# Optimization experiments

Hardware: AMD Instinct MI355X
Metric: run time of the kernel (lower is better)

## Reference

```python
import jax, jax.numpy as jnp
import numpy as np

T, B, IN = 2048, 64, 256
H, L = 256, 3


def setup_inputs() -> dict:
    key = jax.random.key(0)
    ks = jax.random.split(key, 6)
    s = 1.0 / np.sqrt(H)  # torch default init scale
    return {
        "x": jax.random.normal(ks[0], (T, B, IN), dtype=jnp.float32),
        "h0": jax.random.normal(ks[1], (L, B, H), dtype=jnp.float32),
        "W_ih": jax.random.normal(ks[2], (L, 3 * H, IN), dtype=jnp.float32) * s,
        "W_hh": jax.random.normal(ks[3], (L, 3 * H, H), dtype=jnp.float32) * s,
        "b_ih": jax.random.normal(ks[4], (L, 3 * H), dtype=jnp.float32) * s,
        "b_hh": jax.random.normal(ks[5], (L, 3 * H), dtype=jnp.float32) * s,
    }


def _gru_layer(x, h0_l, Wih, Whh, bih, bhh):
    # Precompute input projections for all timesteps: [T, B, 3H]
    gx = jnp.einsum("tbi,gi->tbg", x, Wih) + bih

    def step(h, gx_t):
        gh = h @ Whh.T + bhh  # [B, 3H]
        xr, xz, xn = jnp.split(gx_t, 3, axis=-1)
        hr, hz, hn = jnp.split(gh, 3, axis=-1)
        r = jax.nn.sigmoid(xr + hr)
        z = jax.nn.sigmoid(xz + hz)
        n = jnp.tanh(xn + r * hn)
        h_new = (1.0 - z) * n + z * h
        return h_new, h_new

    hT, out = jax.lax.scan(step, h0_l, gx)
    return out, hT  # out: [T, B, H]


def reference(x, h0, W_ih, W_hh, b_ih, b_hh):
    inp = x
    h_n = []
    for l in range(L):
        inp, hT = _gru_layer(inp, h0[l], W_ih[l], W_hh[l], b_ih[l], b_hh[l])
        h_n.append(hT)
    return inp, jnp.stack(h_n, axis=0)
```

## Files before the change

kernel.cpp:

```cpp
#include <hip/hip_runtime.h>


typedef float  float4_  __attribute__((ext_vector_type(4)));
typedef short  short8_  __attribute__((ext_vector_type(8)));

#define DEVFN static __device__ __forceinline__

constexpr int T_ = 2048;
constexpr int B_ = 64;
constexpr int H_ = 256;
constexpr int G_ = 768;

DEVFN unsigned short f2bf(float f) {
  unsigned u = __float_as_uint(f);
  u += 0x7fffu + ((u >> 16) & 1u);
  return (unsigned short)(u >> 16);
}
DEVFN float bf2f(unsigned short s) { return __uint_as_float(((unsigned)s) << 16); }
DEVFN float rcp_(float x)  { return __builtin_amdgcn_rcpf(x); }
DEVFN float exp2_(float x) { return __builtin_amdgcn_exp2f(x); }
DEVFN float sigmoid_(float x) { return rcp_(1.f + exp2_(-1.4426950408889634f * x)); }
DEVFN float tanh_(float x)    { return 1.f - 2.f * rcp_(1.f + exp2_(2.8853900817779268f * x)); }

DEVFN void load_lds16(const void* g, void* l) {
  __builtin_amdgcn_global_load_lds(
      (__attribute__((address_space(1))) void*)g,
      (__attribute__((address_space(3))) void*)l, 16, 0, 0);
}

__global__ void convert_kernel(const float* __restrict__ x,
                               const float* __restrict__ wih,
                               const float* __restrict__ whh,
                               const float* __restrict__ bih,
                               const float* __restrict__ bhh,
                               unsigned short* __restrict__ xb,
                               unsigned short* __restrict__ wihb,
                               unsigned short* __restrict__ whhb,
                               float* __restrict__ biasf,
                               float* __restrict__ bhhn) {
  const long i0 = (long)blockIdx.x * blockDim.x + threadIdx.x;
  const long stride = (long)gridDim.x * blockDim.x;
  for (long i = i0; i < (long)T_ * B_ * H_; i += stride) xb[i] = f2bf(x[i]);
  for (long i = i0; i < 3L * G_ * H_; i += stride) {
    wihb[i] = f2bf(wih[i]);
    whhb[i] = f2bf(whh[i]);
  }
  for (long i = i0; i < 3L * G_; i += stride) {
    int g = (int)(i % G_);
    biasf[i] = bih[i] + (g < 512 ? bhh[i] : 0.f);
  }
  for (long i = i0; i < 3L * H_; i += stride) {
    int l = (int)(i >> 8), j = (int)(i & 255);
    bhhn[i] = bhh[l * G_ + 512 + j];
  }
}

__global__ __launch_bounds__(256) void gemm_gx(const unsigned short* __restrict__ A,
                                               const unsigned short* __restrict__ W,
                                               const float* __restrict__ bias,
                                               unsigned short* __restrict__ gxrz,
                                               float* __restrict__ gxn) {
  __shared__ alignas(16) unsigned short As[128 * 32];
  __shared__ alignas(16) unsigned short Bs[128 * 32];
  const int tid = threadIdx.x;
  const int bn = blockIdx.x;
  const size_t bm = blockIdx.y;
  const int wave = tid >> 6, lane = tid & 63;
  const int q = lane >> 4, nl = lane & 15;
  const int wr = (wave >> 1) * 64, wc = (wave & 1) * 64;
  const unsigned short* Ab = A + bm * 128 * 256;
  const unsigned short* Wb = W + (size_t)bn * 128 * 256;

  float4_ acc[4][4];
  float4_ z4 = {0.f, 0.f, 0.f, 0.f};
#pragma unroll
  for (int i = 0; i < 4; ++i)
#pragma unroll
    for (int j = 0; j < 4; ++j) acc[i][j] = z4;

  for (int kt = 0; kt < 8; ++kt) {
    const int k0 = kt * 32;
#pragma unroll
    for (int cc = 0; cc < 2; ++cc) {
      int ch = tid + 256 * cc;
      load_lds16(Ab + (size_t)(ch >> 2) * 256 + k0 + (ch & 3) * 8, &As[ch * 8]);
      load_lds16(Wb + (size_t)(ch >> 2) * 256 + k0 + (ch & 3) * 8, &Bs[ch * 8]);
    }
    __syncthreads();
    short8_ af[4], bf[4];
#pragma unroll
    for (int i = 0; i < 4; ++i) {
      af[i] = *(const short8_*)&As[(wr + i * 16 + nl) * 32 + q * 8];
      bf[i] = *(const short8_*)&Bs[(wc + i * 16 + nl) * 32 + q * 8];
    }
#pragma unroll
    for (int i = 0; i < 4; ++i)
#pragma unroll
      for (int j = 0; j < 4; ++j)
        acc[i][j] = __builtin_amdgcn_mfma_f32_16x16x32_bf16(af[i], bf[j], acc[i][j], 0, 0, 0);
    __syncthreads();
  }

  float bv[4];
#pragma unroll
  for (int j = 0; j < 4; ++j) bv[j] = bias[bn * 128 + wc + j * 16 + nl];

  if (bn < 4) {
#pragma unroll
    for (int i = 0; i < 4; ++i)
#pragma unroll
      for (int j = 0; j < 4; ++j) {
        const int gcol = bn * 128 + wc + j * 16 + nl;
#pragma unroll
        for (int r = 0; r < 4; ++r) {
          const size_t grow = bm * 128 + wr + i * 16 + q * 4 + r;
          gxrz[grow * 512 + gcol] = f2bf(acc[i][j][r] + bv[j]);
        }
      }
  } else {
#pragma unroll
    for (int i = 0; i < 4; ++i)
#pragma unroll
      for (int j = 0; j < 4; ++j) {
        const int gcol = bn * 128 + wc + j * 16 + nl;
#pragma unroll
        for (int r = 0; r < 4; ++r) {
          const size_t grow = bm * 128 + wr + i * 16 + q * 4 + r;
          gxn[grow * 256 + (gcol - 512)] = acc[i][j][r] + bv[j];
        }
      }
  }
}

__global__ __launch_bounds__(512, 2) void gru_layer(
    const unsigned short* __restrict__ gxrz,
    const float* __restrict__ gxn,
    const unsigned short* __restrict__ whh,
    const float* __restrict__ bhhn,
    const float* __restrict__ h0,
    unsigned short* __restrict__ outb,
    float* __restrict__ outf,
    float* __restrict__ hT) {
  __shared__ alignas(16) unsigned short h_bf[16][264];
  __shared__ float h_f[16][256];
  __shared__ alignas(16) unsigned short srz[16 * 512];
  __shared__ alignas(16) float sn[16 * 256];

  const int tid = threadIdx.x;
  const int rb = blockIdx.x * 16;
  const int wave = tid >> 6, lane = tid & 63;
  const int q = lane >> 4, nl = lane & 15;
  const int cb = wave * 32;

#pragma unroll
  for (int i = 0; i < 8; ++i) {
    int idx = tid + 512 * i, row = idx >> 8, col = idx & 255;
    float v = h0[(rb + row) * 256 + col];
    h_f[row][col] = v;
    h_bf[row][col] = f2bf(v);
  }

  short8_ wf[6][8];
#pragma unroll
  for (int c = 0; c < 2; ++c)
#pragma unroll
    for (int g = 0; g < 3; ++g) {
      const unsigned short* wrow = whh + (size_t)(g * 256 + cb + c * 16 + nl) * 256;
#pragma unroll
      for (int kt = 0; kt < 8; ++kt)
        wf[c * 3 + g][kt] = *(const short8_*)(wrow + kt * 32 + q * 8);
    }
  const float bn_[2] = { bhhn[cb + nl], bhhn[cb + 16 + nl] };

  {
    const unsigned short* s0 = gxrz + (size_t)rb * 512;
    const float* s1 = gxn + (size_t)rb * 256;
#pragma unroll
    for (int cc = 0; cc < 2; ++cc) {
      int ch = tid + 512 * cc;
      load_lds16(s0 + ch * 8, &srz[ch * 8]);
      load_lds16(s1 + ch * 4, &sn[ch * 4]);
    }
  }
  __syncthreads();

  for (int t = 0; t < T_; ++t) {
    float4_ acc[6];
    float4_ z4 = {0.f, 0.f, 0.f, 0.f};
#pragma unroll
    for (int u = 0; u < 6; ++u) acc[u] = z4;
#pragma unroll
    for (int kt = 0; kt < 8; ++kt) {
      short8_ af = *(const short8_*)&h_bf[nl][kt * 32 + q * 8];
#pragma unroll
      for (int u = 0; u < 6; ++u)
        acc[u] = __builtin_amdgcn_mfma_f32_16x16x32_bf16(af, wf[u][kt], acc[u], 0, 0, 0);
    }
    __syncthreads();

    float hnew[2][4];
#pragma unroll
    for (int c = 0; c < 2; ++c) {
      const int col = cb + c * 16 + nl;
#pragma unroll
      for (int r = 0; r < 4; ++r) {
        const int row = q * 4 + r;
        float xr = bf2f(srz[row * 512 + col]);
        float xz = bf2f(srz[row * 512 + 256 + col]);
        float xn = sn[row * 256 + col];
        float rr = sigmoid_(xr + acc[c * 3 + 0][r]);
        float zz = sigmoid_(xz + acc[c * 3 + 1][r]);
        float nn = tanh_(xn + rr * (acc[c * 3 + 2][r] + bn_[c]));
        float hold = h_f[row][col];
        float hv = nn + zz * (hold - nn);
        hnew[c][r] = hv;
        h_f[row][col] = hv;
        h_bf[row][col] = f2bf(hv);
      }
    }
    __syncthreads();

    const size_t ob = ((size_t)t * 64 + rb) * 256;
    if (outb) {
#pragma unroll
      for (int c = 0; c < 2; ++c)
#pragma unroll
        for (int r = 0; r < 4; ++r)
          outb[ob + (size_t)(q * 4 + r) * 256 + cb + c * 16 + nl] = f2bf(hnew[c][r]);
    }
    if (outf) {
#pragma unroll
      for (int c = 0; c < 2; ++c)
#pragma unroll
        for (int r = 0; r < 4; ++r)
          outf[ob + (size_t)(q * 4 + r) * 256 + cb + c * 16 + nl] = hnew[c][r];
    }
    if (t + 1 < T_) {
      const unsigned short* s0 = gxrz + ((size_t)(t + 1) * 64 + rb) * 512;
      const float* s1 = gxn + ((size_t)(t + 1) * 64 + rb) * 256;
#pragma unroll
      for (int cc = 0; cc < 2; ++cc) {
        int ch = tid + 512 * cc;
        load_lds16(s0 + ch * 8, &srz[ch * 8]);
        load_lds16(s1 + ch * 4, &sn[ch * 4]);
      }
    }
  }

#pragma unroll
  for (int i = 0; i < 8; ++i) {
    int idx = tid + 512 * i, row = idx >> 8, col = idx & 255;
    hT[(rb + row) * 256 + col] = h_f[row][col];
  }
}

extern "C" void kernel_launch(void* const* d_in, const int* in_sizes, int n_in,
                              void* d_out, int out_size, void* d_ws, size_t ws_size,
                              hipStream_t stream) {
  (void)in_sizes; (void)n_in; (void)out_size; (void)ws_size;
  const float* x   = (const float*)d_in[0];
  const float* h0  = (const float*)d_in[1];
  const float* wih = (const float*)d_in[2];
  const float* whh = (const float*)d_in[3];
  const float* bih = (const float*)d_in[4];
  const float* bhh = (const float*)d_in[5];
  float* out = (float*)d_out;
  char* ws = (char*)d_ws;

  unsigned short* gxrz = (unsigned short*)(ws + 0);
  float*          gxn  = (float*)(ws + 134217728);
  unsigned short* buf0 = (unsigned short*)(ws + 268435456);
  unsigned short* buf1 = (unsigned short*)(ws + 335544320);
  unsigned short* wihb = (unsigned short*)(ws + 402653184);
  unsigned short* whhb = (unsigned short*)(ws + 403832832);
  float*         biasf = (float*)(ws + 405012480);
  float*          bhhn = (float*)(ws + 405021696);

  convert_kernel<<<2048, 256, 0, stream>>>(x, wih, whh, bih, bhh,
                                           buf0, wihb, whhb, biasf, bhhn);

  for (int l = 0; l < 3; ++l) {
    const unsigned short* inb = (l & 1) ? buf1 : buf0;
    unsigned short* outbuf    = (l & 1) ? buf0 : buf1;
    gemm_gx<<<dim3(6, 1024), 256, 0, stream>>>(inb, wihb + (size_t)l * G_ * H_,
                                               biasf + l * G_, gxrz, gxn);
    gru_layer<<<4, 512, 0, stream>>>(
        gxrz, gxn, whhb + (size_t)l * G_ * H_, bhhn + l * H_,
        h0 + (size_t)l * B_ * H_,
        (l < 2) ? outbuf : (unsigned short*)nullptr,
        (l == 2) ? out : (float*)nullptr,
        out + (size_t)T_ * B_ * H_ + (size_t)l * B_ * H_);
  }
}
```

Baseline: 19.64 ms.

## Double-buffer hidden state and prefetch gate inputs into registers per step

The recurrent kernel drops the LDS staging of the precomputed input gates. Each thread now loads its own r/z (interleaved bf16 pair) and n values straight into registers one step ahead, and the GEMM epilogue writes r and z interleaved to match. The hidden state is kept in registers for the fp32 path, and the bf16 copy in LDS is double-buffered, which cuts the per-step barriers from two to one and removes the h_f LDS array. The cost is more registers per thread and reliance on the register prefetch arriving in time, which could limit occupancy at 512 threads.

Measured after the change: 36.42 ms. 85.4% more time.

```diff
diff --git a/kernel.cpp b/kernel.cpp
--- a/kernel.cpp
+++ b/kernel.cpp
@@ -111,10 +111,12 @@
 #pragma unroll
       for (int j = 0; j < 4; ++j) {
         const int gcol = bn * 128 + wc + j * 16 + nl;
+        const int g = gcol >> 8;
+        const int col = gcol & 255;
 #pragma unroll
         for (int r = 0; r < 4; ++r) {
           const size_t grow = bm * 128 + wr + i * 16 + q * 4 + r;
-          gxrz[grow * 512 + gcol] = f2bf(acc[i][j][r] + bv[j]);
+          gxrz[grow * 512 + col * 2 + g] = f2bf(acc[i][j][r] + bv[j]);
         }
       }
   } else {
@@ -131,6 +133,52 @@
       }
   }
 }
+
+
+#define GRU_PREFETCH(RZ, XN, tt)                                              \
+  if ((tt) < T_) {                                                            \
+    const unsigned* prz = (const unsigned*)gxrz + (size_t)(tt) * 16384;       \
+    const float* pxn = gxn + (size_t)(tt) * 16384;                            \
+    _Pragma("unroll") for (int c = 0; c < 2; ++c)                             \
+    _Pragma("unroll") for (int r = 0; r < 4; ++r) {                           \
+      RZ[c * 4 + r] = prz[off_[c][r]];                                        \
+      XN[c * 4 + r] = pxn[off_[c][r]];                                        \
+    }                                                                         \
+  }
+
+#define GRU_STEP(RZ, XN, RZN, XNN, t)                                         \
+  {                                                                           \
+    __syncthreads();         \
+    float4_ acc[6];                                                           \
+    _Pragma("unroll") for (int u = 0; u < 6; ++u) acc[u] = z4;                \
+    GRU_PREFETCH(RZN, XNN, (t) + 1);                                          \
+    const unsigned short* hb = &h_bf[((t) + 1) & 1][0][0];                    \
+    _Pragma("unroll") for (int kt = 0; kt < 8; ++kt) {                        \
+      short8_ af = *(const short8_*)&hb[nl * 264 + kt * 32 + q * 8];          \
+      _Pragma("unroll") for (int u = 0; u < 6; ++u)                           \
+        acc[u] =                                                              \
+            __builtin_amdgcn_mfma_f32_16x16x32_bf16(af, wf[u][kt], acc[u], 0, 0, 0); \
+    }                                                                         \
+    unsigned short* hw = &h_bf[(t) & 1][0][0];                                \
+    const size_t ob = ((size_t)(t) * 64 + rb) * 256;                          \
+    _Pragma("unroll") for (int c = 0; c < 2; ++c) {                           \
+      const int col = cb + c * 16 + nl;                                       \
+      _Pragma("unroll") for (int r = 0; r < 4; ++r) {                         \
+        const int row = q * 4 + r;                                            \
+        const unsigned rzv = RZ[c * 4 + r];                                   \
+        const float xr = bf2f((unsigned short)(rzv & 0xffffu));               \
+        const float xz = bf2f((unsigned short)(rzv >> 16));                   \
+        const float rr = sigmoid_(xr + acc[c * 3 + 0][r]);                    \
+        const float zz = sigmoid_(xz + acc[c * 3 + 1][r]);                    \
+        const float nn = tanh_(XN[c * 4 + r] + rr * (acc[c * 3 + 2][r] + bn_[c])); \
+        const float hv = nn + zz * (hold[c][r] - nn);                         \
+        hold[c][r] = hv;                                                      \
+        hw[row * 264 + col] = f2bf(hv);                                       \
+        if (outb) outb[ob + (size_t)row * 256 + col] = f2bf(hv);              \
+        if (outf) outf[ob + (size_t)row * 256 + col] = hv;                    \
+      }                                                                       \
+    }                                                                         \
+  }
 
 __global__ __launch_bounds__(512, 2) void gru_layer(
     const unsigned short* __restrict__ gxrz,
@@ -141,24 +189,14 @@
     unsigned short* __restrict__ outb,
     float* __restrict__ outf,
     float* __restrict__ hT) {
-  __shared__ alignas(16) unsigned short h_bf[16][264];
-  __shared__ float h_f[16][256];
-  __shared__ alignas(16) unsigned short srz[16 * 512];
-  __shared__ alignas(16) float sn[16 * 256];
+  __shared__ alignas(16) unsigned short h_bf[2][16][264];
 
   const int tid = threadIdx.x;
   const int rb = blockIdx.x * 16;
   const int wave = tid >> 6, lane = tid & 63;
   const int q = lane >> 4, nl = lane & 15;
   const int cb = wave * 32;
-
-#pragma unroll
-  for (int i = 0; i < 8; ++i) {
-    int idx = tid + 512 * i, row = idx >> 8, col = idx & 255;
-    float v = h0[(rb + row) * 256 + col];
-    h_f[row][col] = v;
-    h_bf[row][col] = f2bf(v);
-  }
+  const float4_ z4 = {0.f, 0.f, 0.f, 0.f};
 
   short8_ wf[6][8];
 #pragma unroll
@@ -172,86 +210,38 @@
     }
   const float bn_[2] = { bhhn[cb + nl], bhhn[cb + 16 + nl] };
 
-  {
-    const unsigned short* s0 = gxrz + (size_t)rb * 512;
-    const float* s1 = gxn + (size_t)rb * 256;
-#pragma unroll
-    for (int cc = 0; cc < 2; ++cc) {
-      int ch = tid + 512 * cc;
-      load_lds16(s0 + ch * 8, &srz[ch * 8]);
-      load_lds16(s1 + ch * 4, &sn[ch * 4]);
-    }
-  }
-  __syncthreads();
-
-  for (int t = 0; t < T_; ++t) {
-    float4_ acc[6];
-    float4_ z4 = {0.f, 0.f, 0.f, 0.f};
-#pragma unroll
-    for (int u = 0; u < 6; ++u) acc[u] = z4;
-#pragma unroll
-    for (int kt = 0; kt < 8; ++kt) {
-      short8_ af = *(const short8_*)&h_bf[nl][kt * 32 + q * 8];
-#pragma unroll
-      for (int u = 0; u < 6; ++u)
-        acc[u] = __builtin_amdgcn_mfma_f32_16x16x32_bf16(af, wf[u][kt], acc[u], 0, 0, 0);
-    }
-    __syncthreads();
-
-    float hnew[2][4];
-#pragma unroll
-    for (int c = 0; c < 2; ++c) {
-      const int col = cb + c * 16 + nl;
-#pragma unroll
-      for (int r = 0; r < 4; ++r) {
-        const int row = q * 4 + r;
-        float xr = bf2f(srz[row * 512 + col]);
-        float xz = bf2f(srz[row * 512 + 256 + col]);
-        float xn = sn[row * 256 + col];
-        float rr = sigmoid_(xr + acc[c * 3 + 0][r]);
-        float zz = sigmoid_(xz + acc[c * 3 + 1][r]);
-        float nn = tanh_(xn + rr * (acc[c * 3 + 2][r] + bn_[c]));
-        float hold = h_f[row][col];
-        float hv = nn + zz * (hold - nn);
-        hnew[c][r] = hv;
-        h_f[row][col] = hv;
-        h_bf[row][col] = f2bf(hv);
-      }
-    }
-    __syncthreads();
-
-    const size_t ob = ((size_t)t * 64 + rb) * 256;
-    if (outb) {
-#pragma unroll
-      for (int c = 0; c < 2; ++c)
-#pragma unroll
-        for (int r = 0; r < 4; ++r)
-          outb[ob + (size_t)(q * 4 + r) * 256 + cb + c * 16 + nl] = f2bf(hnew[c][r]);
-    }
-    if (outf) {
-#pragma unroll
-      for (int c = 0; c < 2; ++c)
-#pragma unroll
-        for (int r = 0; r < 4; ++r)
-          outf[ob + (size_t)(q * 4 + r) * 256 + cb + c * 16 + nl] = hnew[c][r];
-    }
-    if (t + 1 < T_) {
-      const unsigned short* s0 = gxrz + ((size_t)(t + 1) * 64 + rb) * 512;
-      const float* s1 = gxn + ((size_t)(t + 1) * 64 + rb) * 256;
-#pragma unroll
-      for (int cc = 0; cc < 2; ++cc) {
-        int ch = tid + 512 * cc;
-        load_lds16(s0 + ch * 8, &srz[ch * 8]);
-        load_lds16(s1 + ch * 4, &sn[ch * 4]);
-      }
-    }
-  }
-
-#pragma unroll
-  for (int i = 0; i < 8; ++i) {
-    int idx = tid + 512 * i, row = idx >> 8, col = idx & 255;
-    hT[(rb + row) * 256 + col] = h_f[row][col];
-  }
+  int off_[2][4];
+#pragma unroll
+  for (int c = 0; c < 2; ++c)
+#pragma unroll
+    for (int r = 0; r < 4; ++r)
+      off_[c][r] = (rb + q * 4 + r) * 256 + (cb + c * 16 + nl);
+
+  float hold[2][4];
+#pragma unroll
+  for (int c = 0; c < 2; ++c)
+#pragma unroll
+    for (int r = 0; r < 4; ++r) {
+      const int row = q * 4 + r, col = cb + c * 16 + nl;
+      const float v = h0[(rb + row) * 256 + col];
+      hold[c][r] = v;
+      h_bf[1][row][col] = f2bf(v);
+    }
+
+  unsigned rzA[8], rzB[8];
+  float xnA[8], xnB[8];
+  GRU_PREFETCH(rzA, xnA, 0);
+
+  for (int t = 0; t < T_; t += 2) {
+    GRU_STEP(rzA, xnA, rzB, xnB, t);
+    GRU_STEP(rzB, xnB, rzA, xnA, t + 1);
+  }
+
+#pragma unroll
+  for (int c = 0; c < 2; ++c)
+#pragma unroll
+    for (int r = 0; r < 4; ++r)
+      hT[(rb + q * 4 + r) * 256 + cb + c * 16 + nl] = hold[c][r];
 }
 
 extern "C" void kernel_launch(void* const* d_in, const int* in_sizes, int n_in,
```
